# Kernel optimization log

Measured on AMD Instinct MI355X. Metric: run time of the kernel, lower is better.

The kernel has to match this reference:

```python
import jax, jax.numpy as jnp
import numpy as np

B, CIN, IMG = 8, 512, 112
P = IMG // 14          # patch_size = 8
NP = 14 * 14           # n_patch = 196
DEC, SKIP, EMB = 512, 512, 768
BN_EPS = 1e-3          # keras BatchNormalization default
IN_EPS = 1e-3          # tfa InstanceNormalization default


def conv2d(x, w, b, stride=1):
    # x: NCHW, w: OIHW
    y = jax.lax.conv_general_dilated(x, w, (stride, stride), 'VALID',
                                     dimension_numbers=('NCHW', 'OIHW', 'NCHW'))
    return y + b[None, :, None, None]


def bn_inf(x, g, b, m, v):
    scale = g / jnp.sqrt(v + BN_EPS)
    return (x - m[None, :, None, None]) * scale[None, :, None, None] + b[None, :, None, None]


def setup_inputs() -> dict:
    key = jax.random.key(0)
    ks = jax.random.split(key, 20)
    s = 0.05
    return {
        'decoder': jax.random.normal(ks[0], (B, CIN, IMG, IMG), jnp.float32),
        'trans': jax.random.normal(ks[1], (B, NP, EMB), jnp.float32),
        'pe_w': jax.random.normal(ks[2], (DEC, CIN, P, P), jnp.float32) * s,
        'pe_b': jax.random.normal(ks[3], (DEC,), jnp.float32) * s,
        'mc_w': jax.random.normal(ks[4], (SKIP, CIN, 1, 1), jnp.float32) * s,
        'mc_b': jax.random.normal(ks[5], (SKIP,), jnp.float32) * s,
        'bn1_g': jax.random.uniform(ks[6], (SKIP,), jnp.float32, 0.5, 1.5),
        'bn1_b': jax.random.normal(ks[7], (SKIP,), jnp.float32) * s,
        'bn1_m': jax.random.normal(ks[8], (SKIP,), jnp.float32) * s,
        'bn1_v': jax.random.uniform(ks[9], (SKIP,), jnp.float32, 0.5, 1.5),
        'wq': jax.random.normal(ks[10], (DEC, SKIP), jnp.float32) * s,
        'wk': jax.random.normal(ks[11], (EMB, SKIP), jnp.float32) * s,
        'wv': jax.random.normal(ks[12], (EMB, SKIP), jnp.float32) * s,
        'wo': jax.random.normal(ks[13], (SKIP, SKIP), jnp.float32) * s,
        'psi_g': jnp.ones((1,), jnp.float32),
        'psi_b': jnp.zeros((1,), jnp.float32),
        'rc_w': jax.random.normal(ks[14], (SKIP, SKIP, 1, 1), jnp.float32) * s,
        'rc_b': jax.random.normal(ks[15], (SKIP,), jnp.float32) * s,
        'bn2_g': jax.random.uniform(ks[16], (SKIP,), jnp.float32, 0.5, 1.5),
        'bn2_b': jax.random.normal(ks[17], (SKIP,), jnp.float32) * s,
        'bn2_m': jax.random.normal(ks[18], (SKIP,), jnp.float32) * s,
        'bn2_v': jax.random.uniform(ks[19], (SKIP,), jnp.float32, 0.5, 1.5),
    }


def reference(decoder, trans, pe_w, pe_b, mc_w, mc_b, bn1_g, bn1_b, bn1_m, bn1_v,
              wq, wk, wv, wo, psi_g, psi_b, rc_w, rc_b, bn2_g, bn2_b, bn2_m, bn2_v):
    # mask branch: 1x1 conv + BN + ReLU  -> [B, SKIP, IMG, IMG]
    mask = jax.nn.relu(bn_inf(conv2d(decoder, mc_w, mc_b), bn1_g, bn1_b, bn1_m, bn1_v))

    # patch embedding: strided conv -> [B, DEC, 14, 14] -> tokens [B, NP, DEC]
    dl = conv2d(decoder, pe_w, pe_b, stride=P)
    dl = dl.reshape(dl.shape[0], dl.shape[1], -1).transpose(0, 2, 1)

    q = jnp.einsum('bnd,ds->bsn', dl, wq)       # [B, SKIP, NP]
    k = jnp.einsum('bne,es->bns', trans, wk)    # [B, NP, SKIP]
    v = jnp.einsum('bne,es->bsn', trans, wv)    # [B, SKIP, NP]

    sim = jnp.einsum('bsn,bnt->bst', q, k)      # [B, SKIP, SKIP]
    # InstanceNorm over the (SKIP, SKIP) map per sample (single channel)
    mu = sim.mean(axis=(1, 2), keepdims=True)
    var = sim.var(axis=(1, 2), keepdims=True)
    sim = (sim - mu) / jnp.sqrt(var + IN_EPS) * psi_g[0] + psi_b[0]
    sim = jax.nn.softmax(sim, axis=-1)

    out = jnp.einsum('bst,btn->bns', sim, v)    # [B, NP, SKIP]
    out = jnp.einsum('bns,so->bno', out, wo)    # [B, NP, SKIP]

    # reconstruct: tokens -> [B, SKIP, 14, 14] -> nearest upsample x P -> 1x1 conv + BN + ReLU
    x = out.transpose(0, 2, 1).reshape(out.shape[0], SKIP, 14, 14)
    x = jnp.repeat(jnp.repeat(x, P, axis=2), P, axis=3)
    x = jax.nn.relu(bn_inf(conv2d(x, rc_w, rc_b), bn2_g, bn2_b, bn2_m, bn2_v))

    return x * mask
```

## Files before the change

kernel.cpp:

```cpp
#include <hip/hip_runtime.h>
#include <stdint.h>

typedef __attribute__((ext_vector_type(8))) short v8s;
typedef __attribute__((ext_vector_type(4))) float v4f;

__device__ __forceinline__ uint16_t f2bf(float x){
  uint32_t u = __float_as_uint(x);
  return (uint16_t)((u + 0x7FFFu + ((u >> 16) & 1u)) >> 16);
}
__device__ __forceinline__ uint32_t pk2(float a, float b){
  return (uint32_t)f2bf(a) | ((uint32_t)f2bf(b) << 16);
}
__device__ __forceinline__ int swz(int e){ return e ^ (((e >> 7) & 3) << 3); }

__device__ __forceinline__ void gl16(const uint16_t* g, uint16_t* l){
  __builtin_amdgcn_global_load_lds((const __attribute__((address_space(1))) void*)g,
                                   (__attribute__((address_space(3))) void*)l, 16, 0, 0);
}

__global__ void __launch_bounds__(256) dra_cvt(const float* __restrict__ s,
                                               uint16_t* __restrict__ d, int n8){
  int i = blockIdx.x * 256 + threadIdx.x;
  if (i >= n8) return;
  const float4* sp = (const float4*)(s + (size_t)i * 8);
  float4 f0 = sp[0], f1 = sp[1];
  uint4 u; u.x = pk2(f0.x, f0.y); u.y = pk2(f0.z, f0.w);
  u.z = pk2(f1.x, f1.y); u.w = pk2(f1.z, f1.w);
  *(uint4*)(d + (size_t)i * 8) = u;
}

__global__ void __launch_bounds__(256) dra_tcvt(const float* __restrict__ s,
                                                uint16_t* __restrict__ d, int R, int C){
  int r8 = R >> 3;
  int id = blockIdx.x * 256 + threadIdx.x;
  if (id >= C * r8) return;
  int c = id / r8, r0 = (id - c * r8) * 8;
  float v[8];
  #pragma unroll
  for (int e = 0; e < 8; e++) v[e] = s[(size_t)(r0 + e) * C + c];
  uint4 u; u.x = pk2(v[0], v[1]); u.y = pk2(v[2], v[3]);
  u.z = pk2(v[4], v[5]); u.w = pk2(v[6], v[7]);
  *(uint4*)(d + (size_t)c * R + r0) = u;
}

__global__ void __launch_bounds__(256) dra_tdec(const float* __restrict__ dec,
                                                uint16_t* __restrict__ decT){
  __shared__ uint16_t lt[64 * 80];
  int t = threadIdx.x;
  int pos0 = blockIdx.x * 64;
  int ci0  = blockIdx.y * 64;
  int b    = blockIdx.z;
  #pragma unroll
  for (int i = 0; i < 4; i++){
    int idx = t + i * 256;
    int ci_l = idx >> 4, p4 = (idx & 15) * 4;
    const float4 f = *(const float4*)(dec + ((size_t)(b * 512 + ci0 + ci_l)) * 12544 + pos0 + p4);
    lt[(p4 + 0) * 80 + ci_l] = f2bf(f.x);
    lt[(p4 + 1) * 80 + ci_l] = f2bf(f.y);
    lt[(p4 + 2) * 80 + ci_l] = f2bf(f.z);
    lt[(p4 + 3) * 80 + ci_l] = f2bf(f.w);
  }
  __syncthreads();
  #pragma unroll
  for (int i = 0; i < 2; i++){
    int idx = t + i * 256;
    int p_l = idx >> 3, u = idx & 7;
    uint4 v = *(const uint4*)&lt[p_l * 80 + u * 8];
    *(uint4*)(decT + ((size_t)b * 12544 + pos0 + p_l) * 512 + ci0 + u * 8) = v;
  }
}

__global__ void __launch_bounds__(256) dra_wpe2(const float* __restrict__ pw,
                                                uint16_t* __restrict__ w2){
  int id = blockIdx.x * 256 + threadIdx.x;
  if (id >= 2097152) return;
  int co = id >> 12, rem = id & 4095;
  int ci8 = rem >> 6, pix = rem & 63;
  const float* s = pw + (size_t)co * 32768 + ci8 * 512 + pix;
  float v[8];
  #pragma unroll
  for (int j = 0; j < 8; j++) v[j] = s[j * 64];
  uint4 u; u.x = pk2(v[0], v[1]); u.y = pk2(v[2], v[3]);
  u.z = pk2(v[4], v[5]); u.w = pk2(v[6], v[7]);
  *(uint4*)(w2 + (size_t)co * 32768 + pix * 512 + ci8 * 8) = u;
}

__global__ void __launch_bounds__(256) dra_transb(const float* __restrict__ tr,
                                                  uint16_t* __restrict__ d){
  int id = blockIdx.x * 256 + threadIdx.x;
  if (id >= 1792 * 96) return;
  int n = id / 96, e0 = (id - n * 96) * 8;
  int b = n / 224, nl = n - b * 224;
  uint4 u = {0u,0u,0u,0u};
  if (nl < 196){
    const float* sp = tr + ((size_t)(b * 196 + nl)) * 768 + e0;
    u.x = pk2(sp[0], sp[1]); u.y = pk2(sp[2], sp[3]);
    u.z = pk2(sp[4], sp[5]); u.w = pk2(sp[6], sp[7]);
  }
  *(uint4*)(d + (size_t)n * 768 + e0) = u;
}

__global__ void dra_scales(const float* mcb, const float* g1, const float* b1,
                           const float* m1, const float* v1,
                           const float* rcb, const float* g2, const float* b2,
                           const float* m2, const float* v2,
                           float* s1, float* o1, float* s2, float* o2){
  int i = blockIdx.x * 256 + threadIdx.x;
  if (i >= 512) return;
  float sc1 = g1[i] / sqrtf(v1[i] + 1e-3f);
  s1[i] = sc1; o1[i] = (mcb[i] - m1[i]) * sc1 + b1[i];
  float sc2 = g2[i] / sqrtf(v2[i] + 1e-3f);
  s2[i] = sc2; o2[i] = (rcb[i] - m2[i]) * sc2 + b2[i];
}

__global__ void __launch_bounds__(256, 4) dra_k1(const uint16_t* __restrict__ decT,
    const uint16_t* __restrict__ wpe2, float* __restrict__ part)
{
  __shared__ uint16_t lA[128 * 32];
  __shared__ uint16_t lB[128 * 32];
  int t = threadIdx.x;
  int L = blockIdx.x;
  int x = L & 7, n = L >> 3;
  int shi = n / 56, rem = n - shi * 56;
  int tok_t = rem >> 2, co_t = rem & 3;
  int s    = shi * 8 + x;
  int bco  = co_t * 128;
  int tok0 = tok_t * 128;
  int lane = t & 63, w = t >> 6;
  int wm = w >> 1, wn = w & 1;
  int lr = lane & 15, lg = lane >> 4;

  const uint16_t* aB[2]; const uint16_t* bB[2]; int uu[2];
  #pragma unroll
  for (int i = 0; i < 2; i++){
    int u = t + i * 256; uu[i] = u;
    int row = u >> 2, h = u & 3;
    int token = tok0 + row;
    int b = token / 224, tl = token - b * 224;
    if (tl > 195) tl = 195;
    int py = tl / 14, px = tl - py * 14;
    aB[i] = decT + ((size_t)b * 12544 + py * 896 + px * 8) * 512 + h * 8;
    bB[i] = wpe2 + (size_t)(bco + row) * 32768 + h * 8;
  }

  const v4f vzero = {0.f,0.f,0.f,0.f};
  v4f acc[4][4];
  #pragma unroll
  for (int i = 0; i < 4; i++)
    #pragma unroll
    for (int j = 0; j < 4; j++) acc[i][j] = vzero;

  for (int pix = s * 4; pix < s * 4 + 4; ++pix){
    int ky = pix >> 3, kx = pix & 7;
    int poff = (ky * 112 + kx) * 512;
    int k0p  = pix * 512;
    for (int ci0 = 0; ci0 < 512; ci0 += 32){
      gl16(aB[0] + poff + ci0, &lA[uu[0] * 8]);
      gl16(aB[1] + poff + ci0, &lA[uu[1] * 8]);
      gl16(bB[0] + k0p + ci0,  &lB[uu[0] * 8]);
      gl16(bB[1] + k0p + ci0,  &lB[uu[1] * 8]);
      __syncthreads();
      v8s av[4], bv[4];
      #pragma unroll
      for (int mf = 0; mf < 4; mf++) av[mf] = *(const v8s*)&lA[(wm*64 + mf*16 + lr) * 32 + lg * 8];
      #pragma unroll
      for (int nf = 0; nf < 4; nf++) bv[nf] = *(const v8s*)&lB[(wn*64 + nf*16 + lr) * 32 + lg * 8];
      #pragma unroll
      for (int mf = 0; mf < 4; mf++)
        #pragma unroll
        for (int nf = 0; nf < 4; nf++)
          acc[mf][nf] = __builtin_amdgcn_mfma_f32_16x16x32_bf16(av[mf], bv[nf], acc[mf][nf], 0, 0, 0);
      __syncthreads();
    }
  }
  float* pd = part + (size_t)s * 917504;
  #pragma unroll
  for (int mf = 0; mf < 4; mf++){
    #pragma unroll
    for (int nf = 0; nf < 4; nf++){
      int tokg = tok0 + wm*64 + mf*16 + lg*4;
      int cog  = bco  + wn*64 + nf*16 + lr;
      #pragma unroll
      for (int r = 0; r < 4; r++)
        pd[(size_t)(tokg + r) * 512 + cog] = acc[mf][nf][r];
    }
  }
}

__global__ void __launch_bounds__(256) dra_red(const float* __restrict__ part,
    const float* __restrict__ peb, uint16_t* __restrict__ dlb){
  int id = blockIdx.x * 256 + threadIdx.x;
  if (id >= 114688) return;
  int tok = id >> 6, c8 = (id & 63) * 8;
  float a0=0,a1=0,a2=0,a3=0,a4=0,a5=0,a6=0,a7=0;
  #pragma unroll
  for (int s = 0; s < 16; s++){
    const float* p = part + (size_t)s * 917504 + (size_t)tok * 512 + c8;
    float4 x = *(const float4*)p, y = *(const float4*)(p + 4);
    a0 += x.x; a1 += x.y; a2 += x.z; a3 += x.w;
    a4 += y.x; a5 += y.y; a6 += y.z; a7 += y.w;
  }
  const float4 b0 = *(const float4*)(peb + c8), b1 = *(const float4*)(peb + c8 + 4);
  uint4 o; o.x = pk2(a0 + b0.x, a1 + b0.y); o.y = pk2(a2 + b0.z, a3 + b0.w);
  o.z = pk2(a4 + b1.x, a5 + b1.y); o.w = pk2(a6 + b1.z, a7 + b1.w);
  *(uint4*)(dlb + (size_t)tok * 512 + c8) = o;
}

template<int MREP>
__global__ void __launch_bounds__(256, 2) dra_gemm(
    const uint16_t* __restrict__ A, const uint16_t* __restrict__ Bn, void* __restrict__ Dv,
    int M, int N, int K, int lda, int ldb, int ldd,
    long long sAz, long long sBz, long long sDz,
    int epi, const float* __restrict__ svec, const float* __restrict__ ovec)
{
  constexpr int BM = MREP * 32;
  __shared__ uint16_t lA[BM * 32];
  __shared__ uint16_t lB[64 * 32];
  int t = threadIdx.x, z = blockIdx.z;
  int bm = blockIdx.x * BM, bn = blockIdx.y * 64;
  const uint16_t* Az = A + (size_t)z * sAz;
  const uint16_t* Bz = Bn + (size_t)z * sBz;
  int lane = t & 63, w = t >> 6;
  int wm = w >> 1, wn = w & 1;
  int lr = lane & 15, lg = lane >> 4;
  const v4f vzero = {0.f, 0.f, 0.f, 0.f};
  v4f acc[MREP][2];
  #pragma unroll
  for (int i = 0; i < MREP; i++){ acc[i][0] = vzero; acc[i][1] = vzero; }

  for (int k0 = 0; k0 < K; k0 += 32){
    #pragma unroll
    for (int i = 0; i < MREP/2; i++){
      int idx = t + i * 256;
      int r = idx >> 2, ko = (idx & 3) << 3;
      int rg = bm + r; if (rg >= M) rg = M - 1;
      *(uint4*)&lA[swz(r * 32 + ko)] = *(const uint4*)(Az + (size_t)rg * lda + k0 + ko);
    }
    {
      int r = t >> 2, ko = (t & 3) << 3;
      *(uint4*)&lB[swz(r * 32 + ko)] = *(const uint4*)(Bz + (size_t)(bn + r) * ldb + k0 + ko);
    }
    __syncthreads();
    v8s av[MREP], bv[2];
    #pragma unroll
    for (int mf = 0; mf < MREP; mf++)
      av[mf] = *(const v8s*)&lA[swz((wm*(MREP*16) + mf*16 + lr) * 32 + lg * 8)];
    #pragma unroll
    for (int nf = 0; nf < 2; nf++)
      bv[nf] = *(const v8s*)&lB[swz((wn*32 + nf*16 + lr) * 32 + lg * 8)];
    #pragma unroll
    for (int mf = 0; mf < MREP; mf++)
      #pragma unroll
      for (int nf = 0; nf < 2; nf++)
        acc[mf][nf] = __builtin_amdgcn_mfma_f32_16x16x32_bf16(av[mf], bv[nf], acc[mf][nf], 0, 0, 0);
    __syncthreads();
  }

  #pragma unroll
  for (int mf = 0; mf < MREP; mf++){
    #pragma unroll
    for (int nf = 0; nf < 2; nf++){
      int mg0 = bm + wm*(MREP*16) + mf*16 + lg*4;
      int ng  = bn + wn*32 + nf*16 + lr;
      #pragma unroll
      for (int r = 0; r < 4; r++){
        int mg = mg0 + r;
        if (mg < M){
          float val = acc[mf][nf][r];
          size_t di = (size_t)z * sDz + (size_t)mg * ldd + ng;
          if (epi == 0)      ((float*)Dv)[di] = val;
          else if (epi == 1) ((uint16_t*)Dv)[di] = f2bf(val);
          else ((float*)Dv)[di] = fmaxf(val * svec[mg] + ovec[mg], 0.f);
        }
      }
    }
  }
}

__global__ void __launch_bounds__(256) dra_stats1(const float* __restrict__ sim,
                                                  double* __restrict__ ps){
  __shared__ double d1[256], d2[256];
  int b = blockIdx.y, blk = blockIdx.x, t = threadIdx.x;
  const float* s = sim + (size_t)b * 262144 + (size_t)blk * 2048 + t * 8;
  float4 x = *(const float4*)s, y = *(const float4*)(s + 4);
  double p1 = (double)x.x + x.y + x.z + x.w + y.x + y.y + y.z + y.w;
  double p2 = (double)x.x*x.x + (double)x.y*x.y + (double)x.z*x.z + (double)x.w*x.w
            + (double)y.x*y.x + (double)y.y*y.y + (double)y.z*y.z + (double)y.w*y.w;
  d1[t] = p1; d2[t] = p2;
  __syncthreads();
  for (int o = 128; o > 0; o >>= 1){
    if (t < o){ d1[t] += d1[t + o]; d2[t] += d2[t + o]; }
    __syncthreads();
  }
  if (t == 0){
    ps[(b * 128 + blk) * 2 + 0] = d1[0];
    ps[(b * 128 + blk) * 2 + 1] = d2[0];
  }
}

__global__ void __launch_bounds__(128) dra_stats2(const double* __restrict__ ps,
    const float* __restrict__ psig, const float* __restrict__ psib, float* __restrict__ ac){
  __shared__ double d1[128], d2[128];
  int b = blockIdx.x, t = threadIdx.x;
  d1[t] = ps[(b * 128 + t) * 2 + 0];
  d2[t] = ps[(b * 128 + t) * 2 + 1];
  __syncthreads();
  for (int o = 64; o > 0; o >>= 1){
    if (t < o){ d1[t] += d1[t + o]; d2[t] += d2[t + o]; }
    __syncthreads();
  }
  if (t == 0){
    double mean = d1[0] * (1.0 / 262144.0);
    double var  = d2[0] * (1.0 / 262144.0) - mean * mean;
    float a = psig[0] / (float)sqrt(var + 1e-3);
    ac[b * 2 + 0] = a;
    ac[b * 2 + 1] = psib[0] - (float)mean * a;
  }
}

__global__ void __launch_bounds__(256) dra_soft(const float* __restrict__ sim,
    const float* __restrict__ ac, uint16_t* __restrict__ P){
  int srow = blockIdx.x, b = blockIdx.y, t = threadIdx.x;
  const float* row = sim + (size_t)b * 262144 + (size_t)srow * 512;
  float a = ac[b * 2], c = ac[b * 2 + 1];
  float v0 = row[t] * a + c, v1 = row[t + 256] * a + c;
  __shared__ float red[256];
  red[t] = fmaxf(v0, v1);
  __syncthreads();
  for (int o = 128; o > 0; o >>= 1){
    if (t < o) red[t] = fmaxf(red[t], red[t + o]);
    __syncthreads();
  }
  float m = red[0];
  __syncthreads();
  float e0 = __expf(v0 - m), e1 = __expf(v1 - m);
  red[t] = e0 + e1;
  __syncthreads();
  for (int o = 128; o > 0; o >>= 1){
    if (t < o) red[t] += red[t + o];
    __syncthreads();
  }
  float inv = 1.f / red[0];
  uint16_t* pr = P + (size_t)b * 262144 + (size_t)srow * 512;
  pr[t] = f2bf(e0 * inv); pr[t + 256] = f2bf(e1 * inv);
}

__global__ void __launch_bounds__(512, 2) dra_k3(const uint16_t* __restrict__ decT,
    const uint16_t* __restrict__ mcw, const float* __restrict__ s1,
    const float* __restrict__ o1, const float* __restrict__ recon,
    float* __restrict__ outp)
{
  __shared__ uint16_t lA[2][256 * 32];
  __shared__ uint16_t lB[2][256 * 32];
  int t = threadIdx.x;
  int L = blockIdx.x;
  int x = L & 7, n = L >> 3;
  int co_t = n & 1, q = n >> 1;
  int g = q * 8 + x;
  int bz = g / 49, pt = g - bz * 49;
  int bco  = co_t * 256;
  int pos0 = pt * 256;
  int lane = t & 63, w = t >> 6;
  int wm = w >> 2, wn = w & 3;
  int lr = lane & 15, lg = lane >> 4;

  const uint16_t* aB[2]; const uint16_t* bB[2]; int uu[2];
  #pragma unroll
  for (int i = 0; i < 2; i++){
    int u = t + i * 512; uu[i] = u;
    int row = u >> 2, c = u & 3;
    int cs = c ^ ((row >> 1) & 3);
    aB[i] = mcw  + (size_t)(bco + row) * 512 + cs * 8;
    bB[i] = decT + ((size_t)bz * 12544 + pos0 + row) * 512 + cs * 8;
  }

  const v4f vzero = {0.f,0.f,0.f,0.f};
  v4f acc[8][4];
  #pragma unroll
  for (int i = 0; i < 8; i++)
    #pragma unroll
    for (int j = 0; j < 4; j++) acc[i][j] = vzero;

  auto stage = [&](int kk, int db){
    int ko = kk << 5;
    gl16(aB[0] + ko, &lA[db][uu[0] * 8]);
    gl16(aB[1] + ko, &lA[db][uu[1] * 8]);
    gl16(bB[0] + ko, &lB[db][uu[0] * 8]);
    gl16(bB[1] + ko, &lB[db][uu[1] * 8]);
  };

  int aoff[8], boff[4];
  #pragma unroll
  for (int mf = 0; mf < 8; mf++){
    int R = wm*128 + mf*16 + lr;
    aoff[mf] = R * 32 + (lg ^ ((R >> 1) & 3)) * 8;
  }
  #pragma unroll
  for (int nf = 0; nf < 4; nf++){
    int R = wn*64 + nf*16 + lr;
    boff[nf] = R * 32 + (lg ^ ((R >> 1) & 3)) * 8;
  }

  stage(0, 0);
  __syncthreads();
  int cur = 0;
  for (int kk = 0; kk < 16; ++kk){
    if (kk + 1 < 16) stage(kk + 1, cur ^ 1);
    v8s av[8], bv[4];
    #pragma unroll
    for (int mf = 0; mf < 8; mf++) av[mf] = *(const v8s*)&lA[cur][aoff[mf]];
    #pragma unroll
    for (int nf = 0; nf < 4; nf++) bv[nf] = *(const v8s*)&lB[cur][boff[nf]];
    #pragma unroll
    for (int mf = 0; mf < 8; mf++)
      #pragma unroll
      for (int nf = 0; nf < 4; nf++)
        acc[mf][nf] = __builtin_amdgcn_mfma_f32_16x16x32_bf16(av[mf], bv[nf], acc[mf][nf], 0, 0, 0);
    __syncthreads();
    cur ^= 1;
  }

  #pragma unroll
  for (int mf = 0; mf < 8; mf++){
    #pragma unroll
    for (int r = 0; r < 4; r++){
      int co = bco + wm*128 + mf*16 + lg*4 + r;
      float sc = s1[co], of = o1[co];
      const float* rrow = recon + (size_t)co * 1792 + bz * 224;
      #pragma unroll
      for (int nf = 0; nf < 4; nf++){
        int pos = pos0 + wn*64 + nf*16 + lr;
        int h = pos / 112, wd = pos - h * 112;
        int pcol = (h >> 3) * 14 + (wd >> 3);
        float mask = fmaxf(acc[mf][nf][r] * sc + of, 0.f);
        outp[((size_t)(bz * 512 + co)) * 12544 + pos] = mask * rrow[pcol];
      }
    }
  }
}

extern "C" void kernel_launch(void* const* d_in, const int* in_sizes, int n_in,
                              void* d_out, int out_size, void* d_ws, size_t ws_size,
                              hipStream_t stream) {
  (void)in_sizes; (void)n_in; (void)out_size; (void)ws_size;
  const float* dec   = (const float*)d_in[0];
  const float* trans = (const float*)d_in[1];
  const float* pe_w  = (const float*)d_in[2];
  const float* pe_b  = (const float*)d_in[3];
  const float* mc_w  = (const float*)d_in[4];
  const float* mc_b  = (const float*)d_in[5];
  const float* bn1g  = (const float*)d_in[6];
  const float* bn1b  = (const float*)d_in[7];
  const float* bn1m  = (const float*)d_in[8];
  const float* bn1v  = (const float*)d_in[9];
  const float* wq    = (const float*)d_in[10];
  const float* wk    = (const float*)d_in[11];
  const float* wv    = (const float*)d_in[12];
  const float* wo    = (const float*)d_in[13];
  const float* psig  = (const float*)d_in[14];
  const float* psib  = (const float*)d_in[15];
  const float* rc_w  = (const float*)d_in[16];
  const float* rc_b  = (const float*)d_in[17];
  const float* bn2g  = (const float*)d_in[18];
  const float* bn2b  = (const float*)d_in[19];
  const float* bn2m  = (const float*)d_in[20];
  const float* bn2v  = (const float*)d_in[21];

  char* p = (char*)d_ws;
  auto take = [&](size_t bytes) -> void* {
    void* r = (void*)p; p += (bytes + 255) & ~(size_t)255; return r;
  };
  uint16_t* decT   = (uint16_t*)take((size_t)8 * 12544 * 512 * 2);
  uint16_t* wpe2   = (uint16_t*)take((size_t)512 * 32768 * 2);
  uint16_t* mcw    = (uint16_t*)take((size_t)512 * 512 * 2);
  uint16_t* rcw    = (uint16_t*)take((size_t)512 * 512 * 2);
  uint16_t* wqT    = (uint16_t*)take((size_t)512 * 512 * 2);
  uint16_t* woT    = (uint16_t*)take((size_t)512 * 512 * 2);
  uint16_t* wkT    = (uint16_t*)take((size_t)512 * 768 * 2);
  uint16_t* wvT    = (uint16_t*)take((size_t)512 * 768 * 2);
  uint16_t* transb = (uint16_t*)take((size_t)1792 * 768 * 2);
  float*    s1v    = (float*)take(512 * 4);
  float*    o1v    = (float*)take(512 * 4);
  float*    s2v    = (float*)take(512 * 4);
  float*    o2v    = (float*)take(512 * 4);
  uint16_t* dlb    = (uint16_t*)take((size_t)1792 * 512 * 2);
  uint16_t* Qt     = (uint16_t*)take((size_t)512 * 1792 * 2);
  uint16_t* Kt     = (uint16_t*)take((size_t)512 * 1792 * 2);
  uint16_t* Vb     = (uint16_t*)take((size_t)1792 * 512 * 2);
  float*    ac     = (float*)take(256);
  double*   ps     = (double*)take((size_t)8 * 128 * 2 * 8);
  float*    part   = (float*)take((size_t)16 * 1792 * 512 * 4);
  float*    simb   = part;
  uint16_t* P      = (uint16_t*)(part + 2097152);
  uint16_t* outb   = P + 2097152;
  uint16_t* out2   = outb + 917504;
  float*    recon  = (float*)(out2 + 917504);

  dra_tdec<<<dim3(196, 8, 8), 256, 0, stream>>>(dec, decT);
  dra_wpe2<<<8192, 256, 0, stream>>>(pe_w, wpe2);
  dra_cvt<<<128, 256, 0, stream>>>(mc_w, mcw, 32768);
  dra_cvt<<<128, 256, 0, stream>>>(rc_w, rcw, 32768);
  dra_tcvt<<<128, 256, 0, stream>>>(wq, wqT, 512, 512);
  dra_tcvt<<<192, 256, 0, stream>>>(wk, wkT, 768, 512);
  dra_tcvt<<<192, 256, 0, stream>>>(wv, wvT, 768, 512);
  dra_tcvt<<<128, 256, 0, stream>>>(wo, woT, 512, 512);
  dra_transb<<<672, 256, 0, stream>>>(trans, transb);
  dra_scales<<<2, 256, 0, stream>>>(mc_b, bn1g, bn1b, bn1m, bn1v,
                                    rc_b, bn2g, bn2b, bn2m, bn2v, s1v, o1v, s2v, o2v);

  dra_k1<<<896, 256, 0, stream>>>(decT, wpe2, part);
  dra_red<<<448, 256, 0, stream>>>(part, pe_b, dlb);

  dra_gemm<2><<<dim3(8, 28, 1), 256, 0, stream>>>(wqT, dlb, Qt, 512, 1792, 512,
      512, 512, 1792, 0, 0, 0, 1, nullptr, nullptr);
  dra_gemm<2><<<dim3(8, 28, 1), 256, 0, stream>>>(wkT, transb, Kt, 512, 1792, 768,
      768, 768, 1792, 0, 0, 0, 1, nullptr, nullptr);
  dra_gemm<2><<<dim3(28, 8, 1), 256, 0, stream>>>(transb, wvT, Vb, 1792, 512, 768,
      768, 768, 512, 0, 0, 0, 1, nullptr, nullptr);

  dra_gemm<2><<<dim3(8, 8, 8), 256, 0, stream>>>(Qt, Kt, simb, 512, 512, 224,
      1792, 1792, 512, 224, 224, 262144, 0, nullptr, nullptr);
  dra_stats1<<<dim3(128, 8), 256, 0, stream>>>(simb, ps);
  dra_stats2<<<8, 128, 0, stream>>>(ps, psig, psib, ac);
  dra_soft<<<dim3(512, 8), 256, 0, stream>>>(simb, ac, P);

  dra_gemm<2><<<dim3(4, 8, 8), 256, 0, stream>>>(Vb, P, outb, 224, 512, 512,
      512, 512, 512, 114688, 262144, 114688, 1, nullptr, nullptr);
  dra_gemm<2><<<dim3(28, 8, 1), 256, 0, stream>>>(outb, woT, out2, 1792, 512, 512,
      512, 512, 512, 0, 0, 0, 1, nullptr, nullptr);
  dra_gemm<2><<<dim3(8, 28, 1), 256, 0, stream>>>(rcw, out2, recon, 512, 1792, 512,
      512, 512, 1792, 0, 0, 0, 2, s2v, o2v);

  dra_k3<<<784, 512, 0, stream>>>(decT, mcw, s1v, o1v, recon, (float*)d_out);
}
```

Baseline: 465.3 us.

## Retile mask GEMM to 128x256 blocks and use direct LDS loads in generic GEMM

The final fused mask/output kernel moves from 512-thread blocks with a 256x256 tile to 256-thread blocks with a 128x256 tile, doubling the grid. The swizzle pattern changes, and A fragments are now loaded one at a time inside the MFMA loop to cut register pressure. The generic GEMM drops its register-staged global-to-LDS copies in favour of global_load_lds with precomputed source pointers and an XOR swizzle. The smaller tile lowers register use and could raise occupancy, at the cost of loading the B (decoder) tile twice as often.

```diff
diff --git a/kernel.cpp b/kernel.cpp
--- a/kernel.cpp
+++ b/kernel.cpp
@@ -11,7 +11,6 @@
 __device__ __forceinline__ uint32_t pk2(float a, float b){
   return (uint32_t)f2bf(a) | ((uint32_t)f2bf(b) << 16);
 }
-__device__ __forceinline__ int swz(int e){ return e ^ (((e >> 7) & 3) << 3); }
 
 __device__ __forceinline__ void gl16(const uint16_t* g, uint16_t* l){
   __builtin_amdgcn_global_load_lds((const __attribute__((address_space(1))) void*)g,
@@ -223,6 +222,35 @@
   int lane = t & 63, w = t >> 6;
   int wm = w >> 1, wn = w & 1;
   int lr = lane & 15, lg = lane >> 4;
+
+  const uint16_t* aSrc[MREP/2]; int uuA[MREP/2];
+  #pragma unroll
+  for (int i = 0; i < MREP/2; i++){
+    int u = t + i * 256; uuA[i] = u;
+    int row = u >> 2, c = u & 3;
+    int cs = c ^ (row & 3);
+    int rg = bm + row; if (rg >= M) rg = M - 1;
+    aSrc[i] = Az + (size_t)rg * lda + cs * 8;
+  }
+  const uint16_t* bSrc;
+  {
+    int row = t >> 2, c = t & 3;
+    int cs = c ^ (row & 3);
+    bSrc = Bz + (size_t)(bn + row) * ldb + cs * 8;
+  }
+
+  int aoff[MREP], boff[2];
+  #pragma unroll
+  for (int mf = 0; mf < MREP; mf++){
+    int R = wm*(MREP*16) + mf*16 + lr;
+    aoff[mf] = R * 32 + (lg ^ (R & 3)) * 8;
+  }
+  #pragma unroll
+  for (int nf = 0; nf < 2; nf++){
+    int R = wn*32 + nf*16 + lr;
+    boff[nf] = R * 32 + (lg ^ (R & 3)) * 8;
+  }
+
   const v4f vzero = {0.f, 0.f, 0.f, 0.f};
   v4f acc[MREP][2];
   #pragma unroll
@@ -230,24 +258,15 @@
 
   for (int k0 = 0; k0 < K; k0 += 32){
     #pragma unroll
-    for (int i = 0; i < MREP/2; i++){
-      int idx = t + i * 256;
-      int r = idx >> 2, ko = (idx & 3) << 3;
-      int rg = bm + r; if (rg >= M) rg = M - 1;
-      *(uint4*)&lA[swz(r * 32 + ko)] = *(const uint4*)(Az + (size_t)rg * lda + k0 + ko);
-    }
-    {
-      int r = t >> 2, ko = (t & 3) << 3;
-      *(uint4*)&lB[swz(r * 32 + ko)] = *(const uint4*)(Bz + (size_t)(bn + r) * ldb + k0 + ko);
-    }
+    for (int i = 0; i < MREP/2; i++)
+      gl16(aSrc[i] + k0, &lA[uuA[i] * 8]);
+    gl16(bSrc + k0, &lB[t * 8]);
     __syncthreads();
     v8s av[MREP], bv[2];
     #pragma unroll
-    for (int mf = 0; mf < MREP; mf++)
-      av[mf] = *(const v8s*)&lA[swz((wm*(MREP*16) + mf*16 + lr) * 32 + lg * 8)];
-    #pragma unroll
-    for (int nf = 0; nf < 2; nf++)
-      bv[nf] = *(const v8s*)&lB[swz((wn*32 + nf*16 + lr) * 32 + lg * 8)];
+    for (int mf = 0; mf < MREP; mf++) av[mf] = *(const v8s*)&lA[aoff[mf]];
+    #pragma unroll
+    for (int nf = 0; nf < 2; nf++)    bv[nf] = *(const v8s*)&lB[boff[nf]];
     #pragma unroll
     for (int mf = 0; mf < MREP; mf++)
       #pragma unroll
@@ -345,32 +364,38 @@
   pr[t] = f2bf(e0 * inv); pr[t + 256] = f2bf(e1 * inv);
 }
 
-__global__ void __launch_bounds__(512, 2) dra_k3(const uint16_t* __restrict__ decT,
+__global__ void __launch_bounds__(256, 2) dra_k3(const uint16_t* __restrict__ decT,
     const uint16_t* __restrict__ mcw, const float* __restrict__ s1,
     const float* __restrict__ o1, const float* __restrict__ recon,
     float* __restrict__ outp)
 {
-  __shared__ uint16_t lA[2][256 * 32];
+  __shared__ uint16_t lA[2][128 * 32];
   __shared__ uint16_t lB[2][256 * 32];
   int t = threadIdx.x;
   int L = blockIdx.x;
   int x = L & 7, n = L >> 3;
-  int co_t = n & 1, q = n >> 1;
-  int g = q * 8 + x;
+  int co_t = n & 3, pg = n >> 2;
+  int g = pg * 8 + x;
   int bz = g / 49, pt = g - bz * 49;
-  int bco  = co_t * 256;
+  int bco  = co_t * 128;
   int pos0 = pt * 256;
-  int lane = t & 63, w = t >> 6;
-  int wm = w >> 2, wn = w & 3;
+  int lane = t & 63, wn = t >> 6;
   int lr = lane & 15, lg = lane >> 4;
 
-  const uint16_t* aB[2]; const uint16_t* bB[2]; int uu[2];
+  const uint16_t* aB[2];
   #pragma unroll
   for (int i = 0; i < 2; i++){
-    int u = t + i * 512; uu[i] = u;
+    int u = t + i * 256;
     int row = u >> 2, c = u & 3;
-    int cs = c ^ ((row >> 1) & 3);
-    aB[i] = mcw  + (size_t)(bco + row) * 512 + cs * 8;
+    int cs = c ^ (row & 3);
+    aB[i] = mcw + (size_t)(bco + row) * 512 + cs * 8;
+  }
+  const uint16_t* bB[4];
+  #pragma unroll
+  for (int i = 0; i < 4; i++){
+    int u = t + i * 256;
+    int row = u >> 2, c = u & 3;
+    int cs = c ^ (row & 3);
     bB[i] = decT + ((size_t)bz * 12544 + pos0 + row) * 512 + cs * 8;
   }
 
@@ -383,22 +408,23 @@
 
   auto stage = [&](int kk, int db){
     int ko = kk << 5;
-    gl16(aB[0] + ko, &lA[db][uu[0] * 8]);
-    gl16(aB[1] + ko, &lA[db][uu[1] * 8]);
-    gl16(bB[0] + ko, &lB[db][uu[0] * 8]);
-    gl16(bB[1] + ko, &lB[db][uu[1] * 8]);
+    gl16(aB[0] + ko, &lA[db][(t      ) * 8]);
+    gl16(aB[1] + ko, &lA[db][(t + 256) * 8]);
+    #pragma unroll
+    for (int i = 0; i < 4; i++)
+      gl16(bB[i] + ko, &lB[db][(t + i * 256) * 8]);
   };
 
   int aoff[8], boff[4];
   #pragma unroll
   for (int mf = 0; mf < 8; mf++){
-    int R = wm*128 + mf*16 + lr;
-    aoff[mf] = R * 32 + (lg ^ ((R >> 1) & 3)) * 8;
+    int R = mf*16 + lr;
+    aoff[mf] = R * 32 + (lg ^ (R & 3)) * 8;
   }
   #pragma unroll
   for (int nf = 0; nf < 4; nf++){
     int R = wn*64 + nf*16 + lr;
-    boff[nf] = R * 32 + (lg ^ ((R >> 1) & 3)) * 8;
+    boff[nf] = R * 32 + (lg ^ (R & 3)) * 8;
   }
 
   stage(0, 0);
@@ -406,16 +432,16 @@
   int cur = 0;
   for (int kk = 0; kk < 16; ++kk){
     if (kk + 1 < 16) stage(kk + 1, cur ^ 1);
-    v8s av[8], bv[4];
-    #pragma unroll
-    for (int mf = 0; mf < 8; mf++) av[mf] = *(const v8s*)&lA[cur][aoff[mf]];
+    v8s bv[4];
     #pragma unroll
     for (int nf = 0; nf < 4; nf++) bv[nf] = *(const v8s*)&lB[cur][boff[nf]];
     #pragma unroll
-    for (int mf = 0; mf < 8; mf++)
+    for (int mf = 0; mf < 8; mf++){
+      v8s av = *(const v8s*)&lA[cur][aoff[mf]];
       #pragma unroll
       for (int nf = 0; nf < 4; nf++)
-        acc[mf][nf] = __builtin_amdgcn_mfma_f32_16x16x32_bf16(av[mf], bv[nf], acc[mf][nf], 0, 0, 0);
+        acc[mf][nf] = __builtin_amdgcn_mfma_f32_16x16x32_bf16(av, bv[nf], acc[mf][nf], 0, 0, 0);
+    }
     __syncthreads();
     cur ^= 1;
   }
@@ -424,7 +450,7 @@
   for (int mf = 0; mf < 8; mf++){
     #pragma unroll
     for (int r = 0; r < 4; r++){
-      int co = bco + wm*128 + mf*16 + lg*4 + r;
+      int co = bco + mf*16 + lg*4 + r;
       float sc = s1[co], of = o1[co];
       const float* rrow = recon + (size_t)co * 1792 + bz * 224;
       #pragma unroll
@@ -531,5 +557,5 @@
   dra_gemm<2><<<dim3(8, 28, 1), 256, 0, stream>>>(rcw, out2, recon, 512, 1792, 512,
       512, 512, 1792, 0, 0, 0, 2, s2v, o2v);
 
-  dra_k3<<<784, 512, 0, stream>>>(decT, mcw, s1v, o1v, recon, (float*)d_out);
-}
+  dra_k3<<<1568, 256, 0, stream>>>(decT, mcw, s1v, o1v, recon, (float*)d_out);
+}
```

Result: faster. 441.7 us (-5.1%).
